# Kernel tuning notes

Hardware: AMD Instinct MI355X
Metric: run time of the kernel (lower is better)

Reference implementation:

```python
import jax, jax.numpy as jnp
import numpy as np
import math

B, T, C = 4, 2048, 2048
H, KVH, D = 16, 4, 128

def _rope(x, inv_freqs):
    # x: [B, h, T, D]; interleaved rotate-half: (-x_odd, x_even)
    x2 = x.reshape(*x.shape[:-1], D // 2, 2)
    rot = jnp.stack([-x2[..., 1], x2[..., 0]], axis=-1).reshape(x.shape)
    return x * jnp.cos(inv_freqs) + rot * jnp.sin(inv_freqs)

def setup_inputs() -> dict:
    key = jax.random.key(0)
    ks = jax.random.split(key, 6)
    x = jax.random.normal(ks[0], (B, T, C), dtype=jnp.float32)
    Wq = jax.random.normal(ks[1], (C, C), dtype=jnp.float32) * (1.0 / math.sqrt(C))
    Wk = jax.random.normal(ks[2], (KVH * D, C), dtype=jnp.float32) * (1.0 / math.sqrt(C))
    Wv = jax.random.normal(ks[3], (KVH * D, C), dtype=jnp.float32) * (1.0 / math.sqrt(C))
    Wo = jax.random.normal(ks[4], (C, C), dtype=jnp.float32) * (1.0 / math.sqrt(C))
    bo = jnp.zeros((C,), dtype=jnp.float32)
    # RoPE angles: theta_{t,i} = t / base^(2i/D), each angle repeated for the pair
    base = 10000.0
    freqs = 1.0 / (base ** (jnp.arange(0, D, 2, dtype=jnp.float32) / D))  # [D/2]
    angles = jnp.arange(T, dtype=jnp.float32)[:, None] * freqs[None, :]   # [T, D/2]
    inv_freqs = jnp.repeat(angles, 2, axis=-1).reshape(1, 1, T, D)
    # additive causal mask
    causal = jnp.tril(jnp.ones((T, T), dtype=bool))
    mask = jnp.where(causal, 0.0, -1e9).astype(jnp.float32).reshape(1, 1, T, T)
    return {"x": x, "start_pos": 0, "inv_freqs": inv_freqs, "mask": mask,
            "Wq": Wq, "Wk": Wk, "Wv": Wv, "Wo": Wo, "bo": bo}

def reference(x, start_pos, inv_freqs, mask, Wq, Wk, Wv, Wo, bo):
    q = (x @ Wq.T).reshape(B, T, H, D).transpose(0, 2, 1, 3)      # [B,H,T,D]
    k = (x @ Wk.T).reshape(B, T, KVH, D).transpose(0, 2, 1, 3)    # [B,KVH,T,D]
    v = (x @ Wv.T).reshape(B, T, KVH, D).transpose(0, 2, 1, 3)
    q = _rope(q, inv_freqs)
    k = _rope(k, inv_freqs)
    # GQA expand (repeat_interleave along head dim)
    rep = H // KVH
    k = jnp.repeat(k, rep, axis=1)
    v = jnp.repeat(v, rep, axis=1)
    attn = jnp.einsum('bhqd,bhkd->bhqk', q, k) * (1.0 / math.sqrt(D)) + mask
    attn = jax.nn.softmax(attn, axis=-1)
    y = jnp.einsum('bhqk,bhkd->bhqd', attn, v)                    # [B,H,T,D]
    y = y.transpose(0, 2, 1, 3).reshape(B, T, C)
    return y @ Wo.T + bo
```

## Files before the change

kernel.cpp:

```cpp
#include <hip/hip_runtime.h>
#include <hip/hip_bf16.h>

typedef __bf16 bf16_t;
typedef __attribute__((ext_vector_type(8))) __bf16 bf16x8;
typedef __attribute__((ext_vector_type(4))) __bf16 bf16x4;
typedef __attribute__((ext_vector_type(4))) float f32x4;

#define NB 4
#define NT 2048
#define NC 2048
#define NH 16
#define NKVH 4
#define ND 128
#define LDQ 2560

__device__ __forceinline__ void gld_lds16(const void* g, void* l) {
  __builtin_amdgcn_global_load_lds((__attribute__((address_space(1))) void*)g,
                                   (__attribute__((address_space(3))) void*)l,
                                   16, 0, 0);
}

__global__ __launch_bounds__(256) void cast_f32_bf16(const float* __restrict__ in,
                                                     bf16_t* __restrict__ out, int n4) {
  int i = blockIdx.x * 256 + threadIdx.x;
  if (i >= n4) return;
  float4 v = ((const float4*)in)[i];
  bf16x4 o = { (__bf16)v.x, (__bf16)v.y, (__bf16)v.z, (__bf16)v.w };
  ((bf16x4*)out)[i] = o;
}

__global__ __launch_bounds__(256) void rope_table(const float* __restrict__ inv_freqs,
                                                  float* __restrict__ ctab,
                                                  float* __restrict__ stab) {
  int i = blockIdx.x * 256 + threadIdx.x;
  int t = i >> 6, p = i & 63;
  float ang = inv_freqs[t * ND + 2 * p];
  ctab[i] = cosf(ang);
  stab[i] = sinf(ang);
}

__global__ __launch_bounds__(256) void rope_apply(bf16_t* __restrict__ qkv,
                                                  const float* __restrict__ ctab,
                                                  const float* __restrict__ stab,
                                                  int col0, int nh, float scale) {
  int idx = blockIdx.x * 256 + threadIdx.x;
  int j = idx & 15;
  int h = (idx >> 4) % nh;
  int row = idx / (16 * nh);
  int t = row & (NT - 1);
  long off = (long)row * LDQ + col0 + h * ND + j * 8;
  bf16x8 v = *(const bf16x8*)(qkv + off);
  f32x4 c = *(const f32x4*)(ctab + t * 64 + j * 4);
  f32x4 s = *(const f32x4*)(stab + t * 64 + j * 4);
  bf16x8 r;
#pragma unroll
  for (int p = 0; p < 4; ++p) {
    float x0 = (float)v[2 * p], x1 = (float)v[2 * p + 1];
    r[2 * p]     = (__bf16)((x0 * c[p] - x1 * s[p]) * scale);
    r[2 * p + 1] = (__bf16)((x1 * c[p] + x0 * s[p]) * scale);
  }
  *(bf16x8*)(qkv + off) = r;
}

template <bool OUT_BF16>
__global__ __launch_bounds__(256) void gemm_bt(const bf16_t* __restrict__ A,
                                               const bf16_t* __restrict__ Bt,
                                               void* __restrict__ Cout,
                                               const float* __restrict__ bias,
                                               int M, int N, int K) {
  __shared__ __align__(16) bf16_t As[128 * 32];
  __shared__ __align__(16) bf16_t Bs[128 * 32];
  const int tid = threadIdx.x;
  const int wid = tid >> 6, lane = tid & 63;
  const int wm = wid >> 1, wn = wid & 1;
  const long am0 = (long)blockIdx.x * 128;
  const long bn0 = (long)blockIdx.y * 128;

  f32x4 acc[4][4] = {};

  const int srow = wid * 32 + (lane >> 2);
  const int skoff = (lane & 3) * 8;
  const bf16_t* ag0 = A + (am0 + srow) * K + skoff;
  const bf16_t* ag1 = A + (am0 + srow + 16) * K + skoff;
  const bf16_t* bg0 = Bt + (bn0 + srow) * K + skoff;
  const bf16_t* bg1 = Bt + (bn0 + srow + 16) * K + skoff;
  bf16_t* al0 = As + (wid * 32) * 32;
  bf16_t* al1 = As + (wid * 32 + 16) * 32;
  bf16_t* bl0 = Bs + (wid * 32) * 32;
  bf16_t* bl1 = Bs + (wid * 32 + 16) * 32;

  const int fr = lane & 15;
  const int fk = (lane >> 4) * 8;
  const bf16_t* afrag = As + (wm * 64 + fr) * 32 + fk;
  const bf16_t* bfrag = Bs + (wn * 64 + fr) * 32 + fk;

  for (int k0 = 0; k0 < K; k0 += 32) {
    gld_lds16(ag0 + k0, al0);
    gld_lds16(ag1 + k0, al1);
    gld_lds16(bg0 + k0, bl0);
    gld_lds16(bg1 + k0, bl1);
    __syncthreads();
    bf16x8 a[4], b[4];
#pragma unroll
    for (int i = 0; i < 4; ++i) a[i] = *(const bf16x8*)(afrag + i * 16 * 32);
#pragma unroll
    for (int i = 0; i < 4; ++i) b[i] = *(const bf16x8*)(bfrag + i * 16 * 32);
#pragma unroll
    for (int mi = 0; mi < 4; ++mi)
#pragma unroll
      for (int ni = 0; ni < 4; ++ni)
        acc[mi][ni] = __builtin_amdgcn_mfma_f32_16x16x32_bf16(a[mi], b[ni], acc[mi][ni], 0, 0, 0);
    __syncthreads();
  }

  const int orow = wm * 64 + ((lane >> 4) << 2);
  const int ocol = wn * 64 + (lane & 15);
#pragma unroll
  for (int mi = 0; mi < 4; ++mi)
#pragma unroll
    for (int ni = 0; ni < 4; ++ni) {
      long col = bn0 + ocol + ni * 16;
#pragma unroll
      for (int r = 0; r < 4; ++r) {
        long row = am0 + orow + mi * 16 + r;
        float vv = acc[mi][ni][r];
        if (OUT_BF16) ((bf16_t*)Cout)[row * N + col] = (__bf16)vv;
        else          ((float*)Cout)[row * N + col] = vv + bias[col];
      }
    }
}

__global__ __launch_bounds__(256) void attn_fwd(const bf16_t* __restrict__ qkv,
                                                const bf16_t* __restrict__ vt,
                                                bf16_t* __restrict__ y) {
  __shared__ __align__(16) bf16_t Kt[2][64 * 128];
  __shared__ __align__(16) bf16_t Vt[2][128 * 64];
  __shared__ __align__(16) bf16_t Pb[4][32 * 64];

  const int tid = threadIdx.x, wid = tid >> 6, lane = tid & 63;
  const int fr = lane & 15, fg = lane >> 4;
  const int bh = blockIdx.y;
  const int b = bh >> 4, h = bh & 15, kvh = h >> 2;
  const int bx = blockIdx.x;
  const long rowbase = (long)b * NT;
  char* PbB = (char*)Pb[wid];

  const bf16_t* ksrc[4];
  const bf16_t* vsrc[4];
#pragma unroll
  for (int i = 0; i < 4; ++i) {
    int kvl = wid * 16 + i * 4 + fg;
    int dbyte = ((lane & 15) * 16) ^ ((kvl & 7) << 4);
    ksrc[i] = qkv + (rowbase + kvl) * (long)LDQ + NC + kvh * ND + (dbyte >> 1);
    int d = wid * 32 + i * 8 + (lane >> 3);
    int kvbyte = ((lane & 7) * 16) ^ ((d & 7) << 4);
    vsrc[i] = vt + (long)(kvh * ND + d) * (NB * NT) + rowbase + (kvbyte >> 1);
  }

  auto STAGE = [&](int buf, int kv0) {
#pragma unroll
    for (int i = 0; i < 4; ++i)
      gld_lds16(ksrc[i] + (long)kv0 * LDQ, &Kt[buf][(wid * 16 + i * 4) * 128]);
#pragma unroll
    for (int i = 0; i < 4; ++i)
      gld_lds16(vsrc[i] + kv0, &Vt[buf][(wid * 32 + i * 8) * 64]);
  };

  int cur = 0;
#pragma unroll 1
  for (int phase = 0; phase < 2; ++phase) {
    const int qt = phase ? (15 - bx) : bx;
    const int q0 = qt * 128;
    const int ntiles = 2 * qt + 2;

    bf16x8 qf[2][4];
#pragma unroll
    for (int mi = 0; mi < 2; ++mi) {
      const bf16_t* qp = qkv + (rowbase + q0 + wid * 32 + mi * 16 + fr) * (long)LDQ + h * ND + fg * 8;
#pragma unroll
      for (int ks = 0; ks < 4; ++ks) qf[mi][ks] = *(const bf16x8*)(qp + ks * 32);
    }

    f32x4 o[2][8] = {};
    float m_st[2][4], l_st[2][4];
#pragma unroll
    for (int mi = 0; mi < 2; ++mi)
#pragma unroll
      for (int r = 0; r < 4; ++r) { m_st[mi][r] = -3e38f; l_st[mi][r] = 0.f; }

    STAGE(cur, 0);
    __syncthreads();

#pragma unroll 1
    for (int t = 0; t < ntiles; ++t) {
      const int kv0 = t * 64;
      if (t + 1 < ntiles) STAGE(cur ^ 1, kv0 + 64);

      const char* KtB = (const char*)Kt[cur];
      const char* VtB = (const char*)Vt[cur];

      f32x4 s[2][4] = {};
#pragma unroll
      for (int ks = 0; ks < 4; ++ks)
#pragma unroll
        for (int ni = 0; ni < 4; ++ni) {
          bf16x8 kb = *(const bf16x8*)(KtB + (ni * 16 + fr) * 256 +
                                       ((ks * 64 + fg * 16) ^ ((fr & 7) << 4)));
          s[0][ni] = __builtin_amdgcn_mfma_f32_16x16x32_bf16(qf[0][ks], kb, s[0][ni], 0, 0, 0);
          s[1][ni] = __builtin_amdgcn_mfma_f32_16x16x32_bf16(qf[1][ks], kb, s[1][ni], 0, 0, 0);
        }

      if (t >= 2 * qt) {
#pragma unroll
        for (int mi = 0; mi < 2; ++mi)
#pragma unroll
          for (int ni = 0; ni < 4; ++ni) {
            int j = kv0 + ni * 16 + fr;
#pragma unroll
            for (int r = 0; r < 4; ++r) {
              int i_ = q0 + wid * 32 + mi * 16 + fg * 4 + r;
              if (j > i_) s[mi][ni][r] = -3e30f;
            }
          }
      }

      float alpha[2][4];
#pragma unroll
      for (int mi = 0; mi < 2; ++mi)
#pragma unroll
        for (int r = 0; r < 4; ++r) {
          float rm = fmaxf(fmaxf(s[mi][0][r], s[mi][1][r]), fmaxf(s[mi][2][r], s[mi][3][r]));
          rm = fmaxf(rm, __shfl_xor(rm, 1));
          rm = fmaxf(rm, __shfl_xor(rm, 2));
          rm = fmaxf(rm, __shfl_xor(rm, 4));
          rm = fmaxf(rm, __shfl_xor(rm, 8));
          float mn = fmaxf(m_st[mi][r], rm);
          alpha[mi][r] = __expf(m_st[mi][r] - mn);
          m_st[mi][r] = mn;
        }
#pragma unroll
      for (int mi = 0; mi < 2; ++mi)
#pragma unroll
        for (int ni = 0; ni < 4; ++ni)
#pragma unroll
          for (int r = 0; r < 4; ++r)
            s[mi][ni][r] = __expf(s[mi][ni][r] - m_st[mi][r]);
#pragma unroll
      for (int mi = 0; mi < 2; ++mi)
#pragma unroll
        for (int r = 0; r < 4; ++r) {
          float t2 = s[mi][0][r] + s[mi][1][r] + s[mi][2][r] + s[mi][3][r];
          t2 += __shfl_xor(t2, 1);
          t2 += __shfl_xor(t2, 2);
          t2 += __shfl_xor(t2, 4);
          t2 += __shfl_xor(t2, 8);
          l_st[mi][r] = l_st[mi][r] * alpha[mi][r] + t2;
        }
#pragma unroll
      for (int mi = 0; mi < 2; ++mi)
#pragma unroll
        for (int n = 0; n < 8; ++n)
#pragma unroll
          for (int r = 0; r < 4; ++r) o[mi][n][r] *= alpha[mi][r];

#pragma unroll
      for (int mi = 0; mi < 2; ++mi)
#pragma unroll
        for (int ni = 0; ni < 4; ++ni)
#pragma unroll
          for (int r = 0; r < 4; ++r) {
            int m = mi * 16 + fg * 4 + r;
            int byte = m * 128 + ((ni * 32 + fr * 2) ^ ((m & 7) << 4));
            *(bf16_t*)(PbB + byte) = (__bf16)s[mi][ni][r];
          }
      bf16x8 pa[2][2];
#pragma unroll
      for (int mi = 0; mi < 2; ++mi)
#pragma unroll
        for (int ks = 0; ks < 2; ++ks) {
          int m = mi * 16 + fr;
          pa[mi][ks] = *(const bf16x8*)(PbB + m * 128 + ((ks * 64 + fg * 16) ^ ((m & 7) << 4)));
        }
#pragma unroll
      for (int ks = 0; ks < 2; ++ks)
#pragma unroll
        for (int n = 0; n < 8; ++n) {
          bf16x8 vb = *(const bf16x8*)(VtB + (n * 16 + fr) * 128 +
                                       ((ks * 64 + fg * 16) ^ ((fr & 7) << 4)));
          o[0][n] = __builtin_amdgcn_mfma_f32_16x16x32_bf16(pa[0][ks], vb, o[0][n], 0, 0, 0);
          o[1][n] = __builtin_amdgcn_mfma_f32_16x16x32_bf16(pa[1][ks], vb, o[1][n], 0, 0, 0);
        }
      __syncthreads();
      cur ^= 1;
    }

#pragma unroll
    for (int mi = 0; mi < 2; ++mi)
#pragma unroll
      for (int r = 0; r < 4; ++r) {
        float rinv = 1.0f / l_st[mi][r];
        long row = rowbase + q0 + wid * 32 + mi * 16 + fg * 4 + r;
#pragma unroll
        for (int n = 0; n < 8; ++n)
          y[row * NC + h * ND + n * 16 + fr] = (__bf16)(o[mi][n][r] * rinv);
      }
  }
}

extern "C" void kernel_launch(void* const* d_in, const int* in_sizes, int n_in,
                              void* d_out, int out_size, void* d_ws, size_t ws_size,
                              hipStream_t stream) {
  const float* x  = (const float*)d_in[0];
  const float* iv = (const float*)d_in[2];
  const float* Wq = (const float*)d_in[4];
  const float* Wk = (const float*)d_in[5];
  const float* Wv = (const float*)d_in[6];
  const float* Wo = (const float*)d_in[7];
  const float* bo = (const float*)d_in[8];
  float* out = (float*)d_out;

  char* ws = (char*)d_ws;
  size_t off = 0;
  auto alloc = [&](size_t bytes) -> void* {
    void* p = ws + off;
    off += (bytes + 255) & ~(size_t)255;
    return p;
  };
  bf16_t* xb   = (bf16_t*)alloc((size_t)NB * NT * NC * 2);
  bf16_t* Wcat = (bf16_t*)alloc((size_t)2560 * 2048 * 2);
  bf16_t* Wvb  = (bf16_t*)alloc((size_t)512 * 2048 * 2);
  bf16_t* Wob  = (bf16_t*)alloc((size_t)2048 * 2048 * 2);
  bf16_t* qkv  = (bf16_t*)alloc((size_t)NB * NT * LDQ * 2);
  bf16_t* vtb  = (bf16_t*)alloc((size_t)512 * NB * NT * 2);
  bf16_t* yb   = (bf16_t*)alloc((size_t)NB * NT * NC * 2);
  float*  ctab = (float*)alloc((size_t)NT * 64 * 4);
  float*  stab = (float*)alloc((size_t)NT * 64 * 4);

  cast_f32_bf16<<<16384, 256, 0, stream>>>(x, xb, 4194304);
  cast_f32_bf16<<<4096, 256, 0, stream>>>(Wq, Wcat, 1048576);
  cast_f32_bf16<<<1024, 256, 0, stream>>>(Wk, Wcat + (size_t)2048 * 2048, 262144);
  cast_f32_bf16<<<1024, 256, 0, stream>>>(Wv, Wvb, 262144);
  cast_f32_bf16<<<4096, 256, 0, stream>>>(Wo, Wob, 1048576);
  rope_table<<<512, 256, 0, stream>>>(iv, ctab, stab);

  gemm_bt<true><<<dim3(64, 20), 256, 0, stream>>>(xb, Wcat, qkv, nullptr, 8192, 2560, 2048);
  gemm_bt<true><<<dim3(4, 64), 256, 0, stream>>>(Wvb, xb, vtb, nullptr, 512, 8192, 2048);

  rope_apply<<<8192, 256, 0, stream>>>(qkv, ctab, stab, 0, NH, 0.08838834764831843f);
  rope_apply<<<2048, 256, 0, stream>>>(qkv, ctab, stab, NC, NKVH, 1.0f);

  attn_fwd<<<dim3(8, 64), 256, 0, stream>>>(qkv, vtb, yb);

  gemm_bt<false><<<dim3(64, 16), 256, 0, stream>>>(yb, Wob, out, bo, 8192, 2048, 2048);
}
```

Measured before the change: 667.3 us.

## Add 256x256 eight-wave pipelined GEMM for QKV and output projections

Introduces a new GEMM kernel with 256x256 block tiles, eight waves and double-buffered 64 KB LDS stages. Global loads go directly to LDS via XOR-swizzled addresses and are issued in interleaved quarter-steps between MFMA phases, with s_setprio raising MFMA priority. It replaces the 128x128 GEMM for the QKV and output projections to raise data reuse and overlap loads with compute. The large LDS footprint limits residency, and the 320-block grid on the QKV projection leaves a partial tail wave.

```diff
diff --git a/kernel.cpp b/kernel.cpp
--- a/kernel.cpp
+++ b/kernel.cpp
@@ -124,6 +124,166 @@
       for (int r = 0; r < 4; ++r) {
         long row = am0 + orow + mi * 16 + r;
         float vv = acc[mi][ni][r];
+        if (OUT_BF16) ((bf16_t*)Cout)[row * N + col] = (__bf16)vv;
+        else          ((float*)Cout)[row * N + col] = vv + bias[col];
+      }
+    }
+}
+
+template <bool OUT_BF16>
+__global__ __launch_bounds__(512, 2) void gemm8p(const bf16_t* __restrict__ A,
+                                                 const bf16_t* __restrict__ Bt,
+                                                 void* __restrict__ Cout,
+                                                 const float* __restrict__ bias,
+                                                 int M, int N, int K) {
+  __shared__ __align__(16) char lds[2][65536];
+  const int tid = threadIdx.x, wid = tid >> 6, lane = tid & 63;
+  const int wm = wid >> 2, wn = wid & 3;
+  const int fr = lane & 15, fg = lane >> 4;
+  const long am0 = (long)blockIdx.x * 256;
+  const long bn0 = (long)blockIdx.y * 256;
+  const long Kl = K;
+  const int NTl = K >> 6;
+
+  const int scol = (((lane & 7) ^ ((lane >> 3) & 7))) * 8;
+  const bf16_t* Ag = A + (am0 + wid * 8 + (lane >> 3)) * Kl + scol;
+  const bf16_t* Bg = Bt + (bn0 + (wid >> 2) * 64 + (wid & 3) * 8 + (lane >> 3)) * Kl + scol;
+  const int abst = wid * 1024 + lane * 16;
+  const int bbst = 32768 + (wid >> 2) * 8192 + (wid & 3) * 1024 + lane * 16;
+
+  const int kx0 = (fg * 16) ^ ((fr & 7) << 4);
+  const int kx1 = kx0 ^ 64;
+  const int abase = wm * 16384 + fr * 128;
+  const int bbase = 32768 + wn * 8192 + fr * 128;
+
+  auto ISSUE = [&](int n) {
+    if (n >= 4 * NTl) return;
+    const int tile = n >> 2;
+    char* l = lds[tile & 1];
+    const long k0 = (long)(tile << 6);
+    switch (n & 3) {
+      case 0:
+        gld_lds16(Ag + k0, l + abst);
+        gld_lds16(Ag + 128 * Kl + k0, l + 16384 + abst);
+        break;
+      case 1:
+        gld_lds16(Bg + k0, l + bbst);
+        gld_lds16(Bg + 128 * Kl + k0, l + 16384 + bbst);
+        break;
+      case 2:
+        gld_lds16(Bg + 32 * Kl + k0, l + 4096 + bbst);
+        gld_lds16(Bg + 160 * Kl + k0, l + 20480 + bbst);
+        break;
+      default:
+        gld_lds16(Ag + 64 * Kl + k0, l + 8192 + abst);
+        gld_lds16(Ag + 192 * Kl + k0, l + 24576 + abst);
+    }
+  };
+
+  f32x4 acc[8][4] = {};
+  bf16x8 a[4][2], b0[2][2], b1[2][2];
+
+  for (int n = 0; n < 7; ++n) ISSUE(n);
+  asm volatile("s_waitcnt vmcnt(6)" ::: "memory");
+  __builtin_amdgcn_s_barrier();
+
+#pragma unroll 1
+  for (int t = 0; t < NTl; ++t) {
+    const char* l = lds[t & 1];
+    const int base = t << 2;
+
+#pragma unroll
+    for (int mi = 0; mi < 4; ++mi) {
+      a[mi][0] = *(const bf16x8*)(l + abase + mi * 2048 + kx0);
+      a[mi][1] = *(const bf16x8*)(l + abase + mi * 2048 + kx1);
+    }
+#pragma unroll
+    for (int nj = 0; nj < 2; ++nj) {
+      b0[nj][0] = *(const bf16x8*)(l + bbase + nj * 2048 + kx0);
+      b0[nj][1] = *(const bf16x8*)(l + bbase + nj * 2048 + kx1);
+    }
+    ISSUE(base + 7);
+    __builtin_amdgcn_s_barrier();
+    asm volatile("s_waitcnt lgkmcnt(0)" ::: "memory");
+    __builtin_amdgcn_sched_barrier(0);
+    __builtin_amdgcn_s_setprio(1);
+#pragma unroll
+    for (int mi = 0; mi < 4; ++mi)
+#pragma unroll
+      for (int nj = 0; nj < 2; ++nj) {
+        acc[mi][nj] = __builtin_amdgcn_mfma_f32_16x16x32_bf16(a[mi][0], b0[nj][0], acc[mi][nj], 0, 0, 0);
+        acc[mi][nj] = __builtin_amdgcn_mfma_f32_16x16x32_bf16(a[mi][1], b0[nj][1], acc[mi][nj], 0, 0, 0);
+      }
+    __builtin_amdgcn_s_setprio(0);
+    __builtin_amdgcn_s_barrier();
+
+#pragma unroll
+    for (int nj = 0; nj < 2; ++nj) {
+      b1[nj][0] = *(const bf16x8*)(l + bbase + (2 + nj) * 2048 + kx0);
+      b1[nj][1] = *(const bf16x8*)(l + bbase + (2 + nj) * 2048 + kx1);
+    }
+    ISSUE(base + 8);
+    __builtin_amdgcn_s_barrier();
+    asm volatile("s_waitcnt lgkmcnt(0)" ::: "memory");
+    __builtin_amdgcn_sched_barrier(0);
+    __builtin_amdgcn_s_setprio(1);
+#pragma unroll
+    for (int mi = 0; mi < 4; ++mi)
+#pragma unroll
+      for (int nj = 0; nj < 2; ++nj) {
+        acc[mi][2 + nj] = __builtin_amdgcn_mfma_f32_16x16x32_bf16(a[mi][0], b1[nj][0], acc[mi][2 + nj], 0, 0, 0);
+        acc[mi][2 + nj] = __builtin_amdgcn_mfma_f32_16x16x32_bf16(a[mi][1], b1[nj][1], acc[mi][2 + nj], 0, 0, 0);
+      }
+    __builtin_amdgcn_s_setprio(0);
+    __builtin_amdgcn_s_barrier();
+
+#pragma unroll
+    for (int mi = 0; mi < 4; ++mi) {
+      a[mi][0] = *(const bf16x8*)(l + abase + 8192 + mi * 2048 + kx0);
+      a[mi][1] = *(const bf16x8*)(l + abase + 8192 + mi * 2048 + kx1);
+    }
+    ISSUE(base + 9);
+    __builtin_amdgcn_s_barrier();
+    asm volatile("s_waitcnt lgkmcnt(0)" ::: "memory");
+    __builtin_amdgcn_sched_barrier(0);
+    __builtin_amdgcn_s_setprio(1);
+#pragma unroll
+    for (int mi = 0; mi < 4; ++mi)
+#pragma unroll
+      for (int nj = 0; nj < 2; ++nj) {
+        acc[4 + mi][2 + nj] = __builtin_amdgcn_mfma_f32_16x16x32_bf16(a[mi][0], b1[nj][0], acc[4 + mi][2 + nj], 0, 0, 0);
+        acc[4 + mi][2 + nj] = __builtin_amdgcn_mfma_f32_16x16x32_bf16(a[mi][1], b1[nj][1], acc[4 + mi][2 + nj], 0, 0, 0);
+      }
+    __builtin_amdgcn_s_setprio(0);
+    __builtin_amdgcn_s_barrier();
+
+    ISSUE(base + 10);
+    if (t < NTl - 2)      asm volatile("s_waitcnt vmcnt(6)" ::: "memory");
+    else                  asm volatile("s_waitcnt vmcnt(0)" ::: "memory");
+    __builtin_amdgcn_s_barrier();
+    asm volatile("s_waitcnt lgkmcnt(0)" ::: "memory");
+    __builtin_amdgcn_sched_barrier(0);
+    __builtin_amdgcn_s_setprio(1);
+#pragma unroll
+    for (int mi = 0; mi < 4; ++mi)
+#pragma unroll
+      for (int nj = 0; nj < 2; ++nj) {
+        acc[4 + mi][nj] = __builtin_amdgcn_mfma_f32_16x16x32_bf16(a[mi][0], b0[nj][0], acc[4 + mi][nj], 0, 0, 0);
+        acc[4 + mi][nj] = __builtin_amdgcn_mfma_f32_16x16x32_bf16(a[mi][1], b0[nj][1], acc[4 + mi][nj], 0, 0, 0);
+      }
+    __builtin_amdgcn_s_setprio(0);
+    __builtin_amdgcn_s_barrier();
+  }
+
+#pragma unroll
+  for (int mi = 0; mi < 8; ++mi)
+#pragma unroll
+    for (int nj = 0; nj < 4; ++nj) {
+      long col = bn0 + wn * 64 + nj * 16 + fr;
+#pragma unroll
+      for (int r = 0; r < 4; ++r) {
+        long row = am0 + wm * 128 + mi * 16 + fg * 4 + r;
+        float vv = acc[mi][nj][r];
         if (OUT_BF16) ((bf16_t*)Cout)[row * N + col] = (__bf16)vv;
         else          ((float*)Cout)[row * N + col] = vv + bias[col];
       }
@@ -343,7 +503,7 @@
   cast_f32_bf16<<<4096, 256, 0, stream>>>(Wo, Wob, 1048576);
   rope_table<<<512, 256, 0, stream>>>(iv, ctab, stab);
 
-  gemm_bt<true><<<dim3(64, 20), 256, 0, stream>>>(xb, Wcat, qkv, nullptr, 8192, 2560, 2048);
+  gemm8p<true><<<dim3(32, 10), 512, 0, stream>>>(xb, Wcat, qkv, nullptr, 8192, 2560, 2048);
   gemm_bt<true><<<dim3(4, 64), 256, 0, stream>>>(Wvb, xb, vtb, nullptr, 512, 8192, 2048);
 
   rope_apply<<<8192, 256, 0, stream>>>(qkv, ctab, stab, 0, NH, 0.08838834764831843f);
@@ -351,5 +511,5 @@
 
   attn_fwd<<<dim3(8, 64), 256, 0, stream>>>(qkv, vtb, yb);
 
-  gemm_bt<false><<<dim3(64, 16), 256, 0, stream>>>(yb, Wob, out, bo, 8192, 2048, 2048);
-}
+  gemm8p<false><<<dim3(32, 8), 512, 0, stream>>>(yb, Wob, out, bo, 8192, 2048, 2048);
+}
```

New measurement: 635.3 us. 1.05x faster.
